# Optimization experiments

Hardware: AMD Instinct MI355X
Metric: run time of the kernel (lower is better)

Reference implementation:

```python
import jax, jax.numpy as jnp
import numpy as np

B, T, VOCAB_SZ, N_SPK = 64, 1024, 34, 128
D_TXT, D_SPK, H, N_MELS = 512, 64, 256, 80


def _lstm_params(key, in_dim, hid):
    k1, k2, k3, k4 = jax.random.split(key, 4)
    s = 1.0 / np.sqrt(hid)
    Wih = jax.random.uniform(k1, (4 * hid, in_dim), jnp.float32, -s, s)
    Whh = jax.random.uniform(k2, (4 * hid, hid), jnp.float32, -s, s)
    bih = jax.random.uniform(k3, (4 * hid,), jnp.float32, -s, s)
    bhh = jax.random.uniform(k4, (4 * hid,), jnp.float32, -s, s)
    return Wih, Whh, bih, bhh


def setup_inputs() -> dict:
    key = jax.random.key(0)
    ks = jax.random.split(key, 10)
    text_seq = jax.random.randint(ks[0], (B, T), 0, VOCAB_SZ)
    mel_spectrogram = jax.random.normal(ks[1], (B, T, N_MELS), jnp.float32)
    speaker_id = jax.random.randint(ks[2], (B,), 0, N_SPK)
    emb_text = jax.random.normal(ks[3], (VOCAB_SZ, D_TXT), jnp.float32)
    emb_text = emb_text.at[0].set(0.0)  # padding_idx=0
    emb_spk = jax.random.normal(ks[4], (N_SPK, D_SPK), jnp.float32)
    Wih_f, Whh_f, bih_f, bhh_f = _lstm_params(ks[5], D_TXT + D_SPK, H)
    Wih_b, Whh_b, bih_b, bhh_b = _lstm_params(ks[6], D_TXT + D_SPK, H)
    Wih_d, _Whh_d, bih_d, bhh_d = _lstm_params(ks[7], N_MELS + 2 * H, H)
    s = 1.0 / np.sqrt(H)
    Wfc = jax.random.uniform(ks[8], (N_MELS, H), jnp.float32, -s, s)
    bfc = jax.random.uniform(ks[9], (N_MELS,), jnp.float32, -s, s)
    return dict(text_seq=text_seq, mel_spectrogram=mel_spectrogram, speaker_id=speaker_id,
                emb_text=emb_text, emb_spk=emb_spk,
                Wih_f=Wih_f, Whh_f=Whh_f, bih_f=bih_f, bhh_f=bhh_f,
                Wih_b=Wih_b, Whh_b=Whh_b, bih_b=bih_b, bhh_b=bhh_b,
                Wih_d=Wih_d, bih_d=bih_d, bhh_d=bhh_d, Wfc=Wfc, bfc=bfc)


def _lstm_scan(xs, Wih, Whh, bih, bhh, reverse=False):
    # xs: [T, B, D] -> hs: [T, B, H] (PyTorch gate order i,f,g,o)
    nB, hid = xs.shape[1], Whh.shape[1]
    bias = bih + bhh
    def step(carry, x):
        h, c = carry
        g = x @ Wih.T + h @ Whh.T + bias
        i, f, gg, o = jnp.split(g, 4, axis=-1)
        c = jax.nn.sigmoid(f) * c + jax.nn.sigmoid(i) * jnp.tanh(gg)
        h = jax.nn.sigmoid(o) * jnp.tanh(c)
        return (h, c), h
    init = (jnp.zeros((nB, hid), xs.dtype), jnp.zeros((nB, hid), xs.dtype))
    _, hs = jax.lax.scan(step, init, xs, reverse=reverse)
    return hs


def reference(text_seq, mel_spectrogram, speaker_id, emb_text, emb_spk,
              Wih_f, Whh_f, bih_f, bhh_f, Wih_b, Whh_b, bih_b, bhh_b,
              Wih_d, bih_d, bhh_d, Wfc, bfc):
    text_embed = emb_text[text_seq]                       # [B, T, 512]
    spk = jnp.broadcast_to(emb_spk[speaker_id][:, None, :],
                           (text_seq.shape[0], text_seq.shape[1], emb_spk.shape[1]))
    enc_in = jnp.concatenate([text_embed, spk], axis=-1)  # [B, T, 576]
    xs = jnp.transpose(enc_in, (1, 0, 2))                 # time-major [T, B, 576]
    h_fwd = _lstm_scan(xs, Wih_f, Whh_f, bih_f, bhh_f)
    h_bwd = _lstm_scan(xs, Wih_b, Whh_b, bih_b, bhh_b, reverse=True)
    enc_out = jnp.concatenate([h_fwd, h_bwd], axis=-1)    # [T, B, 512]

    max_len = min(mel_spectrogram.shape[1], enc_out.shape[0])
    # Decoder: hidden state is reset (None) every step in the original, so
    # c = sigmoid(i)*tanh(g), h = sigmoid(o)*tanh(c); Whh contributes nothing.
    dbias = bih_d + bhh_d
    def dstep(prev_mel, e_t):
        x = jnp.concatenate([prev_mel, e_t], axis=-1)     # [B, 592]
        g = x @ Wih_d.T + dbias
        i, f, gg, o = jnp.split(g, 4, axis=-1)
        c = jax.nn.sigmoid(i) * jnp.tanh(gg)
        h = jax.nn.sigmoid(o) * jnp.tanh(c)
        out = h @ Wfc.T + bfc
        return out, out
    _, outs = jax.lax.scan(dstep, mel_spectrogram[:, 0, :], enc_out[: max_len - 1])
    return jnp.transpose(outs, (1, 0, 2))                 # [B, max_len-1, 80]
```

## Files before the change

kernel.cpp:

```cpp
#include <hip/hip_runtime.h>
#include <hip/hip_fp16.h>
#include <stdint.h>

#define T_SEQ 1024
#define NB    64
#define VOCAB 34
#define NSPK  128
#define DTXT  512
#define HID   256
#define NMEL  80
#define GROWS 1024
#define DROWS 768

typedef _Float16 f16;
typedef _Float16 f16x2 __attribute__((ext_vector_type(2)));
typedef _Float16 v8h __attribute__((ext_vector_type(8)));
typedef float v4f __attribute__((ext_vector_type(4)));

__device__ __forceinline__ float fdot2f(uint32_t a, uint32_t b, float c) {
  return __builtin_amdgcn_fdot2(__builtin_bit_cast(f16x2, a),
                                __builtin_bit_cast(f16x2, b), c, false);
}
__device__ __forceinline__ float sigm(float x) { return 1.0f / (1.0f + __expf(-x)); }
__device__ __forceinline__ float tanhf_fast(float x) {
  float e = __expf(2.0f * x);
  return 1.0f - 2.0f / (e + 1.0f);
}
__device__ __forceinline__ void bar_vperm() {
  asm volatile("s_waitcnt lgkmcnt(0)\n\ts_barrier" ::: "memory");
  __builtin_amdgcn_sched_barrier(0);
}


__global__ void k_tp(const float* __restrict__ Wf, const float* __restrict__ Wb,
                     const float* __restrict__ emb_text, float* __restrict__ TP) {
  int blk = blockIdx.x; int dir = blk / VOCAB; int v = blk - dir * VOCAB;
  const float* W = dir ? Wb : Wf;
  const float* e = emb_text + (size_t)v * DTXT;
  for (int r = threadIdx.x; r < GROWS; r += 256) {
    const float* wr = W + (size_t)r * 576;
    float a0 = 0, a1 = 0, a2 = 0, a3 = 0;
    for (int d = 0; d < DTXT; d += 4) {
      a0 += e[d] * wr[d];     a1 += e[d+1] * wr[d+1];
      a2 += e[d+2] * wr[d+2]; a3 += e[d+3] * wr[d+3];
    }
    TP[(size_t)(dir * VOCAB + v) * GROWS + r] = (a0 + a1) + (a2 + a3);
  }
}

__global__ void k_sp(const float* __restrict__ Wf, const float* __restrict__ Wb,
                     const float* __restrict__ bihf, const float* __restrict__ bhhf,
                     const float* __restrict__ bihb, const float* __restrict__ bhhb,
                     const float* __restrict__ emb_spk, float* __restrict__ SP) {
  int blk = blockIdx.x; int dir = blk >> 7; int s = blk & 127;
  const float* W  = dir ? Wb : Wf;
  const float* bi = dir ? bihb : bihf;
  const float* bh = dir ? bhhb : bhhf;
  const float* e  = emb_spk + (size_t)s * 64;
  for (int r = threadIdx.x; r < GROWS; r += 256) {
    const float* wr = W + (size_t)r * 576 + 512;
    float acc = bi[r] + bh[r];
    for (int d = 0; d < 64; ++d) acc += e[d] * wr[d];
    SP[(size_t)(dir * NSPK + s) * GROWS + r] = acc;
  }
}

__global__ void k_whh(const float* __restrict__ Whhf, const float* __restrict__ Whhb,
                      f16* __restrict__ WhhH) {
  int idx = blockIdx.x * 256 + threadIdx.x;
  if (idx < 2 * GROWS * HID) {
    int dir = idx >> 18; int rem = idx & (GROWS * HID - 1);
    WhhH[idx] = (f16)(dir ? Whhb[rem] : Whhf[rem]);
  }
}

__global__ void k_decw(const float* __restrict__ Wih_d, const float* __restrict__ bih_d,
                       const float* __restrict__ bhh_d,
                       f16* __restrict__ WmH, f16* __restrict__ WdH, float* __restrict__ dbias) {
  int r = blockIdx.x;
  int src = (r < 256) ? r : (r + 256);
  const float* w = Wih_d + (size_t)src * 592;
  for (int k = threadIdx.x; k < 592; k += 256) {
    float v = w[k];
    if (k < 80) WmH[(size_t)r * 80 + k] = (f16)v;
    else        WdH[(size_t)r * 512 + (k - 80)] = (f16)v;
  }
  if (threadIdx.x == 0) dbias[r] = bih_d[src] + bhh_d[src];
}

__global__ void k_misc(const float* __restrict__ Wfc, f16* __restrict__ WfcH) {
  int idx = blockIdx.x * 256 + threadIdx.x;
  if (idx < NMEL * HID) WfcH[idx] = (f16)Wfc[idx];
}

__launch_bounds__(512, 2)
__global__ void k_enc(const int* __restrict__ text_seq, const int* __restrict__ speaker_id,
                      const float* __restrict__ TP, const float* __restrict__ SP,
                      const uint32_t* __restrict__ WhhH_dw,
                      f16* __restrict__ Hh) {
  __shared__ __align__(16) uint4 wtail[16 * 512];
  __shared__ __align__(16) uint32_t hbuf[2][128];
  __shared__ float pp[4][256];
  __shared__ int tseq[T_SEQ];

  int wg = blockIdx.x;
  int dir = wg >> 6, b = wg & 63;
  int tid = threadIdx.x;
  int u = tid & 255, kh = tid >> 8;

  uint4 w0[12], w1[12], w2[12], w3[12];
  {
    const uint4* p0 = (const uint4*)(WhhH_dw + ((size_t)(dir << 10) + u      ) * 128 + (kh << 6));
    const uint4* p1 = (const uint4*)(WhhH_dw + ((size_t)(dir << 10) + u + 256) * 128 + (kh << 6));
    const uint4* p2 = (const uint4*)(WhhH_dw + ((size_t)(dir << 10) + u + 512) * 128 + (kh << 6));
    const uint4* p3 = (const uint4*)(WhhH_dw + ((size_t)(dir << 10) + u + 768) * 128 + (kh << 6));
    #pragma unroll
    for (int i = 0; i < 12; ++i) { w0[i] = p0[i]; w1[i] = p1[i]; w2[i] = p2[i]; w3[i] = p3[i]; }
    #pragma unroll
    for (int j = 0; j < 4; ++j) {
      wtail[(0 * 4 + j) * 512 + tid] = p0[12 + j];
      wtail[(1 * 4 + j) * 512 + tid] = p1[12 + j];
      wtail[(2 * 4 + j) * 512 + tid] = p2[12 + j];
      wtail[(3 * 4 + j) * 512 + tid] = p3[12 + j];
    }
  }
  for (int i = tid; i < T_SEQ; i += 512) tseq[i] = text_seq[b * T_SEQ + i];
  if (tid < 128) hbuf[0][tid] = 0u;
  float sp0 = 0, sp1 = 0, sp2 = 0, sp3 = 0;
  if (kh == 0) {
    int spk = speaker_id[b];
    sp0 = SP[(size_t)(dir * NSPK + spk) * GROWS + u];
    sp1 = SP[(size_t)(dir * NSPK + spk) * GROWS + u + 256];
    sp2 = SP[(size_t)(dir * NSPK + spk) * GROWS + u + 512];
    sp3 = SP[(size_t)(dir * NSPK + spk) * GROWS + u + 768];
  }
  const float* TPd = TP + (size_t)dir * VOCAB * GROWS;
  float c_state = 0.0f;
  __syncthreads();

  float x0 = 0, x1 = 0, x2 = 0, x3 = 0;
  if (kh == 0) {
    int v = tseq[dir ? (T_SEQ - 1) : 0];
    x0 = TPd[(size_t)v * GROWS + u];
    x1 = TPd[(size_t)v * GROWS + u + 256];
    x2 = TPd[(size_t)v * GROWS + u + 512];
    x3 = TPd[(size_t)v * GROWS + u + 768];
  }

  float h_keep = 0.0f; int t_keep = 0;
  for (int n = 0; n < T_SEQ; ++n) {
    int t = dir ? (T_SEQ - 1 - n) : n;
    float xn0 = 0, xn1 = 0, xn2 = 0, xn3 = 0;
    if (kh == 0) {
      if (n > 0)
        Hh[((size_t)(dir * T_SEQ + t_keep) * NB + b) * HID + u] = (f16)h_keep;
      int tn = dir ? (T_SEQ - 2 - n) : (n + 1);
      tn = tn < 0 ? 0 : (tn > T_SEQ - 1 ? T_SEQ - 1 : tn);
      int vn = tseq[tn];
      xn0 = TPd[(size_t)vn * GROWS + u];
      xn1 = TPd[(size_t)vn * GROWS + u + 256];
      xn2 = TPd[(size_t)vn * GROWS + u + 512];
      xn3 = TPd[(size_t)vn * GROWS + u + 768];
    }

    float i0 = 0, i1 = 0, f0 = 0, f1 = 0, g0 = 0, g1 = 0, o0 = 0, o1 = 0;
    const uint4* h4 = ((const uint4*)hbuf[n & 1]) + (kh << 4);
    #pragma unroll
    for (int c = 0; c < 12; ++c) {
      uint4 hv = h4[c];
      i0 = fdot2f(w0[c].x, hv.x, i0); f0 = fdot2f(w1[c].x, hv.x, f0);
      g0 = fdot2f(w2[c].x, hv.x, g0); o0 = fdot2f(w3[c].x, hv.x, o0);
      i1 = fdot2f(w0[c].y, hv.y, i1); f1 = fdot2f(w1[c].y, hv.y, f1);
      g1 = fdot2f(w2[c].y, hv.y, g1); o1 = fdot2f(w3[c].y, hv.y, o1);
      i0 = fdot2f(w0[c].z, hv.z, i0); f0 = fdot2f(w1[c].z, hv.z, f0);
      g0 = fdot2f(w2[c].z, hv.z, g0); o0 = fdot2f(w3[c].z, hv.z, o0);
      i1 = fdot2f(w0[c].w, hv.w, i1); f1 = fdot2f(w1[c].w, hv.w, f1);
      g1 = fdot2f(w2[c].w, hv.w, g1); o1 = fdot2f(w3[c].w, hv.w, o1);
    }
    #pragma unroll
    for (int j = 0; j < 4; ++j) {
      uint4 hv = h4[12 + j];
      uint4 t0v = wtail[(0 * 4 + j) * 512 + tid];
      uint4 t1v = wtail[(1 * 4 + j) * 512 + tid];
      uint4 t2v = wtail[(2 * 4 + j) * 512 + tid];
      uint4 t3v = wtail[(3 * 4 + j) * 512 + tid];
      i0 = fdot2f(t0v.x, hv.x, i0); f0 = fdot2f(t1v.x, hv.x, f0);
      g0 = fdot2f(t2v.x, hv.x, g0); o0 = fdot2f(t3v.x, hv.x, o0);
      i1 = fdot2f(t0v.y, hv.y, i1); f1 = fdot2f(t1v.y, hv.y, f1);
      g1 = fdot2f(t2v.y, hv.y, g1); o1 = fdot2f(t3v.y, hv.y, o1);
      i0 = fdot2f(t0v.z, hv.z, i0); f0 = fdot2f(t1v.z, hv.z, f0);
      g0 = fdot2f(t2v.z, hv.z, g0); o0 = fdot2f(t3v.z, hv.z, o0);
      i1 = fdot2f(t0v.w, hv.w, i1); f1 = fdot2f(t1v.w, hv.w, f1);
      g1 = fdot2f(t2v.w, hv.w, g1); o1 = fdot2f(t3v.w, hv.w, o1);
    }
    if (kh == 1) {
      pp[0][u] = i0 + i1;
      pp[1][u] = f0 + f1;
      pp[2][u] = g0 + g1;
      pp[3][u] = o0 + o1;
    }
    bar_vperm();

    if (kh == 0) {
      float gi = (i0 + i1) + pp[0][u] + x0 + sp0;
      float gf = (f0 + f1) + pp[1][u] + x1 + sp1;
      float gg = (g0 + g1) + pp[2][u] + x2 + sp2;
      float go = (o0 + o1) + pp[3][u] + x3 + sp3;
      c_state = sigm(gf) * c_state + sigm(gi) * tanhf_fast(gg);
      float h = sigm(go) * tanhf_fast(c_state);
      ((f16*)hbuf[(n + 1) & 1])[u] = (f16)h;
      h_keep = h; t_keep = t;
      x0 = xn0; x1 = xn1; x2 = xn2; x3 = xn3;
    }
    bar_vperm();
  }
  if (kh == 0)
    Hh[((size_t)(dir * T_SEQ + t_keep) * NB + b) * HID + u] = (f16)h_keep;
}

__launch_bounds__(256, 4)
__global__ void k_eproj(const uint32_t* __restrict__ Hdw, const uint32_t* __restrict__ WdH_dw,
                        const float* __restrict__ dbias, f16* __restrict__ E) {
  __shared__ __align__(16) uint32_t Asm[64][68];
  __shared__ __align__(16) uint32_t Wsm[64][68];
  int nt = blockIdx.x % 12;
  int t  = blockIdx.x / 12;
  int n0 = nt * 64;
  int tid = threadIdx.x;
  int wave = tid >> 6, lane = tid & 63;
  int lr = lane & 15, lg = lane >> 4;

  v4f acc0 = {0,0,0,0}, acc1 = {0,0,0,0}, acc2 = {0,0,0,0}, acc3 = {0,0,0,0};

  for (int ch = 0; ch < 4; ++ch) {
    int dirc = ch >> 1, koff = (ch & 1) * 64;
    {
      int bb = tid >> 2, p = tid & 3;
      const uint32_t* asrc = Hdw + ((size_t)(dirc * T_SEQ + t) * NB + bb) * 128 + koff + p * 4;
      const uint32_t* wsrc = WdH_dw + (size_t)(n0 + bb) * 256 + ch * 64 + p * 4;
      #pragma unroll
      for (int q = 0; q < 4; ++q) {
        *(uint4*)(&Asm[bb][p * 4 + q * 16]) = *(const uint4*)(asrc + q * 16);
        *(uint4*)(&Wsm[bb][p * 4 + q * 16]) = *(const uint4*)(wsrc + q * 16);
      }
    }
    __syncthreads();
    #pragma unroll
    for (int sub = 0; sub < 4; ++sub) {
      v8h af = __builtin_bit_cast(v8h, *(const uint4*)&Asm[wave * 16 + lr][sub * 16 + lg * 4]);
      v8h b0 = __builtin_bit_cast(v8h, *(const uint4*)&Wsm[ 0 + lr][sub * 16 + lg * 4]);
      v8h b1 = __builtin_bit_cast(v8h, *(const uint4*)&Wsm[16 + lr][sub * 16 + lg * 4]);
      v8h b2 = __builtin_bit_cast(v8h, *(const uint4*)&Wsm[32 + lr][sub * 16 + lg * 4]);
      v8h b3 = __builtin_bit_cast(v8h, *(const uint4*)&Wsm[48 + lr][sub * 16 + lg * 4]);
      acc0 = __builtin_amdgcn_mfma_f32_16x16x32_f16(af, b0, acc0, 0, 0, 0);
      acc1 = __builtin_amdgcn_mfma_f32_16x16x32_f16(af, b1, acc1, 0, 0, 0);
      acc2 = __builtin_amdgcn_mfma_f32_16x16x32_f16(af, b2, acc2, 0, 0, 0);
      acc3 = __builtin_amdgcn_mfma_f32_16x16x32_f16(af, b3, acc3, 0, 0, 0);
    }
    __syncthreads();
  }

  float db0 = dbias[n0 +  0 + lr];
  float db1 = dbias[n0 + 16 + lr];
  float db2 = dbias[n0 + 32 + lr];
  float db3 = dbias[n0 + 48 + lr];
  #pragma unroll
  for (int reg = 0; reg < 4; ++reg) {
    int m = wave * 16 + lg * 4 + reg;
    f16* Erow = E + ((size_t)t * NB + m) * DROWS + n0;
    Erow[ 0 + lr] = (f16)(acc0[reg] + db0);
    Erow[16 + lr] = (f16)(acc1[reg] + db1);
    Erow[32 + lr] = (f16)(acc2[reg] + db2);
    Erow[48 + lr] = (f16)(acc3[reg] + db3);
  }
}

__launch_bounds__(512, 2)
__global__ void k_dec(const float* __restrict__ mel, const f16* __restrict__ E,
                      const uint32_t* __restrict__ WmH_dw, const uint32_t* __restrict__ WfcH_dw,
                      const float* __restrict__ bfc, float* __restrict__ out) {
  __shared__ __align__(16) uint32_t pm[40];
  __shared__ __align__(16) uint32_t h_sm[128];
  __shared__ float pp[3][256];
  __shared__ __align__(16) uint4 Ebuf[2][16 * 96];

  int b = blockIdx.x;
  int tid = threadIdx.x;
  int u = tid & 255, kh = tid >> 8;

  uint4 wm0[5], wm1[5], wm2[5];
  {
    const uint4* p0 = (const uint4*)(WmH_dw + (size_t)(u      ) * 40) + kh * 5;
    const uint4* p1 = (const uint4*)(WmH_dw + (size_t)(u + 256) * 40) + kh * 5;
    const uint4* p2 = (const uint4*)(WmH_dw + (size_t)(u + 512) * 40) + kh * 5;
    #pragma unroll
    for (int k = 0; k < 5; ++k) { wm0[k] = p0[k]; wm1[k] = p1[k]; wm2[k] = p2[k]; }
  }
  int fr = (tid < 320) ? (tid >> 2) : 0;
  int q  = tid & 3;
  uint4 wfc[8];
  {
    const uint4* wp = (const uint4*)(WfcH_dw + (size_t)fr * 128) + q * 8;
    #pragma unroll
    for (int k = 0; k < 8; ++k) wfc[k] = wp[k];
  }
  float bfcv = bfc[fr];
  if (tid < 40) {
    float m0 = mel[(size_t)b * T_SEQ * NMEL + 2 * tid];
    float m1 = mel[(size_t)b * T_SEQ * NMEL + 2 * tid + 1];
    f16x2 v; v[0] = (f16)m0; v[1] = (f16)m1;
    pm[tid] = __builtin_bit_cast(uint32_t, v);
  }

  int srow = tid >> 5, scol = tid & 31;
  {
    const uint4* src = (const uint4*)(E + ((size_t)srow * NB + b) * DROWS);
    Ebuf[0][srow * 96 + scol     ] = src[scol];
    Ebuf[0][srow * 96 + scol + 32] = src[scol + 32];
    Ebuf[0][srow * 96 + scol + 64] = src[scol + 64];
  }
  __syncthreads();

  float o_keep = 0.0f;
  for (int t = 0; t < T_SEQ - 1; ++t) {
    int w = t >> 4, s = t & 15;
    if (t > 0 && tid < 320 && q == 0)
      out[((size_t)b * (T_SEQ - 1) + (t - 1)) * NMEL + fr] = o_keep;
    uint4 st0, st1, st2;
    bool do_stage = (s == 0) && (w < 63);
    if (do_stage) {
      int rr = (w + 1) * 16 + srow; if (rr > T_SEQ - 2) rr = T_SEQ - 2;
      const uint4* src = (const uint4*)(E + ((size_t)rr * NB + b) * DROWS);
      st0 = src[scol]; st1 = src[scol + 32]; st2 = src[scol + 64];
    }

    float a0 = 0, a1 = 0, a2 = 0;
    const uint4* pm4 = ((const uint4*)pm) + kh * 5;
    #pragma unroll
    for (int k = 0; k < 5; ++k) {
      uint4 hp = pm4[k];
      a0 = fdot2f(wm0[k].x, hp.x, a0); a1 = fdot2f(wm1[k].x, hp.x, a1); a2 = fdot2f(wm2[k].x, hp.x, a2);
      a0 = fdot2f(wm0[k].y, hp.y, a0); a1 = fdot2f(wm1[k].y, hp.y, a1); a2 = fdot2f(wm2[k].y, hp.y, a2);
      a0 = fdot2f(wm0[k].z, hp.z, a0); a1 = fdot2f(wm1[k].z, hp.z, a1); a2 = fdot2f(wm2[k].z, hp.z, a2);
      a0 = fdot2f(wm0[k].w, hp.w, a0); a1 = fdot2f(wm1[k].w, hp.w, a1); a2 = fdot2f(wm2[k].w, hp.w, a2);
    }
    if (kh == 1) { pp[0][u] = a0; pp[1][u] = a1; pp[2][u] = a2; }
    bar_vperm();

    if (kh == 0) {
      const f16* Erow = (const f16*)&Ebuf[w & 1][s * 96];
      float gi = a0 + pp[0][u] + (float)Erow[u];
      float gg = a1 + pp[1][u] + (float)Erow[u + 256];
      float go = a2 + pp[2][u] + (float)Erow[u + 512];
      float cc = sigm(gi) * tanhf_fast(gg);
      float h  = sigm(go) * tanhf_fast(cc);
      ((f16*)h_sm)[u] = (f16)h;
    }
    if (do_stage) {
      Ebuf[(w + 1) & 1][srow * 96 + scol     ] = st0;
      Ebuf[(w + 1) & 1][srow * 96 + scol + 32] = st1;
      Ebuf[(w + 1) & 1][srow * 96 + scol + 64] = st2;
    }
    bar_vperm();

    if (tid < 320) {
      const uint4* hrow = ((const uint4*)h_sm) + q * 8;
      float s0 = 0, s1 = 0, s2 = 0, s3 = 0;
      #pragma unroll
      for (int kk = 0; kk < 8; ++kk) {
        uint4 hq = hrow[kk];
        s0 = fdot2f(wfc[kk].x, hq.x, s0); s1 = fdot2f(wfc[kk].y, hq.y, s1);
        s2 = fdot2f(wfc[kk].z, hq.z, s2); s3 = fdot2f(wfc[kk].w, hq.w, s3);
      }
      float sv = (s0 + s1) + (s2 + s3);
      sv += __shfl_xor(sv, 1);
      sv += __shfl_xor(sv, 2);
      if (q == 0) {
        float o = sv + bfcv;
        o_keep = o;
        ((f16*)pm)[fr] = (f16)o;
      }
    }
    bar_vperm();
  }
  if (tid < 320 && q == 0)
    out[((size_t)b * (T_SEQ - 1) + (T_SEQ - 2)) * NMEL + fr] = o_keep;
}

extern "C" void kernel_launch(void* const* d_in, const int* in_sizes, int n_in,
                              void* d_out, int out_size, void* d_ws, size_t ws_size,
                              hipStream_t stream) {
  const int*   text_seq   = (const int*)d_in[0];
  const float* mel        = (const float*)d_in[1];
  const int*   speaker_id = (const int*)d_in[2];
  const float* emb_text   = (const float*)d_in[3];
  const float* emb_spk    = (const float*)d_in[4];
  const float* Wih_f = (const float*)d_in[5];
  const float* Whh_f = (const float*)d_in[6];
  const float* bih_f = (const float*)d_in[7];
  const float* bhh_f = (const float*)d_in[8];
  const float* Wih_b = (const float*)d_in[9];
  const float* Whh_b = (const float*)d_in[10];
  const float* bih_b = (const float*)d_in[11];
  const float* bhh_b = (const float*)d_in[12];
  const float* Wih_d = (const float*)d_in[13];
  const float* bih_d = (const float*)d_in[14];
  const float* bhh_d = (const float*)d_in[15];
  const float* Wfc   = (const float*)d_in[16];
  const float* bfc   = (const float*)d_in[17];
  float* out = (float*)d_out;

  char* base = (char*)d_ws;
  size_t off = 0;
  auto take = [&](size_t n) -> char* {
    off = (off + 255) & ~(size_t)255;
    char* r = base + off;
    off += n;
    return r;
  };
  float*        TP    = (float*)take((size_t)2 * VOCAB * GROWS * 4);
  float*        SP    = (float*)take((size_t)2 * NSPK * GROWS * 4);
  f16*          WhhH  = (f16*)take((size_t)2 * GROWS * HID * 2);
  f16*          WmH   = (f16*)take((size_t)DROWS * 80 * 2);
  f16*          WdH   = (f16*)take((size_t)DROWS * 512 * 2);
  f16*          WfcH  = (f16*)take((size_t)NMEL * HID * 2);
  float*        dbias = (float*)take((size_t)DROWS * 4);
  f16*          Hh    = (f16*)take((size_t)2 * T_SEQ * NB * HID * 2);
  f16*          E     = (f16*)take((size_t)(T_SEQ - 1) * NB * DROWS * 2);
  if (off > ws_size) return;

  k_tp  <<<2 * VOCAB, 256, 0, stream>>>(Wih_f, Wih_b, emb_text, TP);
  k_sp  <<<2 * NSPK, 256, 0, stream>>>(Wih_f, Wih_b, bih_f, bhh_f, bih_b, bhh_b, emb_spk, SP);
  k_whh <<<2048, 256, 0, stream>>>(Whh_f, Whh_b, WhhH);
  k_decw<<<DROWS, 256, 0, stream>>>(Wih_d, bih_d, bhh_d, WmH, WdH, dbias);
  k_misc<<<80, 256, 0, stream>>>(Wfc, WfcH);
  k_enc <<<128, 512, 0, stream>>>(text_seq, speaker_id, TP, SP,
                                  (const uint32_t*)WhhH, Hh);
  k_eproj<<<(T_SEQ - 1) * 12, 256, 0, stream>>>((const uint32_t*)Hh,
                                                (const uint32_t*)WdH, dbias, E);
  k_dec <<<NB, 512, 0, stream>>>(mel, E, (const uint32_t*)WmH,
                                 (const uint32_t*)WfcH, bfc, out);
}
```

Baseline: 2.846 ms.

## Process two batch rows per decoder block and vectorize input-projection precompute

```diff
diff --git a/kernel.cpp b/kernel.cpp
--- a/kernel.cpp
+++ b/kernel.cpp
@@ -36,13 +36,15 @@
                      const float* __restrict__ emb_text, float* __restrict__ TP) {
   int blk = blockIdx.x; int dir = blk / VOCAB; int v = blk - dir * VOCAB;
   const float* W = dir ? Wb : Wf;
-  const float* e = emb_text + (size_t)v * DTXT;
+  const float4* e4 = (const float4*)(emb_text + (size_t)v * DTXT);
   for (int r = threadIdx.x; r < GROWS; r += 256) {
-    const float* wr = W + (size_t)r * 576;
+    const float4* w4 = (const float4*)(W + (size_t)r * 576);
     float a0 = 0, a1 = 0, a2 = 0, a3 = 0;
-    for (int d = 0; d < DTXT; d += 4) {
-      a0 += e[d] * wr[d];     a1 += e[d+1] * wr[d+1];
-      a2 += e[d+2] * wr[d+2]; a3 += e[d+3] * wr[d+3];
+    #pragma unroll 4
+    for (int d = 0; d < DTXT / 4; ++d) {
+      float4 ev = e4[d], wv = w4[d];
+      a0 += ev.x * wv.x; a1 += ev.y * wv.y;
+      a2 += ev.z * wv.z; a3 += ev.w * wv.w;
     }
     TP[(size_t)(dir * VOCAB + v) * GROWS + r] = (a0 + a1) + (a2 + a3);
   }
@@ -56,12 +58,17 @@
   const float* W  = dir ? Wb : Wf;
   const float* bi = dir ? bihb : bihf;
   const float* bh = dir ? bhhb : bhhf;
-  const float* e  = emb_spk + (size_t)s * 64;
+  const float4* e4 = (const float4*)(emb_spk + (size_t)s * 64);
   for (int r = threadIdx.x; r < GROWS; r += 256) {
-    const float* wr = W + (size_t)r * 576 + 512;
-    float acc = bi[r] + bh[r];
-    for (int d = 0; d < 64; ++d) acc += e[d] * wr[d];
-    SP[(size_t)(dir * NSPK + s) * GROWS + r] = acc;
+    const float4* w4 = (const float4*)(W + (size_t)r * 576 + 512);
+    float a0 = 0, a1 = 0, a2 = 0, a3 = 0;
+    #pragma unroll
+    for (int d = 0; d < 16; ++d) {
+      float4 ev = e4[d], wv = w4[d];
+      a0 += ev.x * wv.x; a1 += ev.y * wv.y;
+      a2 += ev.z * wv.z; a3 += ev.w * wv.w;
+    }
+    SP[(size_t)(dir * NSPK + s) * GROWS + r] = bi[r] + bh[r] + (a0 + a1) + (a2 + a3);
   }
 }
 
@@ -279,22 +286,22 @@
 __global__ void k_dec(const float* __restrict__ mel, const f16* __restrict__ E,
                       const uint32_t* __restrict__ WmH_dw, const uint32_t* __restrict__ WfcH_dw,
                       const float* __restrict__ bfc, float* __restrict__ out) {
-  __shared__ __align__(16) uint32_t pm[40];
-  __shared__ __align__(16) uint32_t h_sm[128];
-  __shared__ float pp[3][256];
-  __shared__ __align__(16) uint4 Ebuf[2][16 * 96];
-
-  int b = blockIdx.x;
+  __shared__ __align__(16) uint32_t pm[2][40];
+  __shared__ __align__(16) uint32_t h_sm[2][128];
+  __shared__ __align__(16) uint4 Ebuf[2][2][16 * 96];
+
+  int b2 = blockIdx.x;
   int tid = threadIdx.x;
-  int u = tid & 255, kh = tid >> 8;
-
-  uint4 wm0[5], wm1[5], wm2[5];
+  int u = tid & 255, hb = tid >> 8;
+  int b = b2 + 32 * hb;
+
+  uint4 wm0[10], wm1[10], wm2[10];
   {
-    const uint4* p0 = (const uint4*)(WmH_dw + (size_t)(u      ) * 40) + kh * 5;
-    const uint4* p1 = (const uint4*)(WmH_dw + (size_t)(u + 256) * 40) + kh * 5;
-    const uint4* p2 = (const uint4*)(WmH_dw + (size_t)(u + 512) * 40) + kh * 5;
-    #pragma unroll
-    for (int k = 0; k < 5; ++k) { wm0[k] = p0[k]; wm1[k] = p1[k]; wm2[k] = p2[k]; }
+    const uint4* p0 = (const uint4*)(WmH_dw + (size_t)(u      ) * 40);
+    const uint4* p1 = (const uint4*)(WmH_dw + (size_t)(u + 256) * 40);
+    const uint4* p2 = (const uint4*)(WmH_dw + (size_t)(u + 512) * 40);
+    #pragma unroll
+    for (int k = 0; k < 10; ++k) { wm0[k] = p0[k]; wm1[k] = p1[k]; wm2[k] = p2[k]; }
   }
   int fr = (tid < 320) ? (tid >> 2) : 0;
   int q  = tid & 3;
@@ -305,86 +312,103 @@
     for (int k = 0; k < 8; ++k) wfc[k] = wp[k];
   }
   float bfcv = bfc[fr];
-  if (tid < 40) {
-    float m0 = mel[(size_t)b * T_SEQ * NMEL + 2 * tid];
-    float m1 = mel[(size_t)b * T_SEQ * NMEL + 2 * tid + 1];
+  if (tid < 80) {
+    int hbi = tid / 40, idx = tid - 40 * hbi;
+    int bb = b2 + 32 * hbi;
+    float m0 = mel[(size_t)bb * T_SEQ * NMEL + 2 * idx];
+    float m1 = mel[(size_t)bb * T_SEQ * NMEL + 2 * idx + 1];
     f16x2 v; v[0] = (f16)m0; v[1] = (f16)m1;
-    pm[tid] = __builtin_bit_cast(uint32_t, v);
+    pm[hbi][idx] = __builtin_bit_cast(uint32_t, v);
   }
 
   int srow = tid >> 5, scol = tid & 31;
-  {
-    const uint4* src = (const uint4*)(E + ((size_t)srow * NB + b) * DROWS);
-    Ebuf[0][srow * 96 + scol     ] = src[scol];
-    Ebuf[0][srow * 96 + scol + 32] = src[scol + 32];
-    Ebuf[0][srow * 96 + scol + 64] = src[scol + 64];
+  #pragma unroll
+  for (int hbs = 0; hbs < 2; ++hbs) {
+    const uint4* src = (const uint4*)(E + ((size_t)srow * NB + b2 + 32 * hbs) * DROWS);
+    Ebuf[0][hbs][srow * 96 + scol     ] = src[scol];
+    Ebuf[0][hbs][srow * 96 + scol + 32] = src[scol + 32];
+    Ebuf[0][hbs][srow * 96 + scol + 64] = src[scol + 64];
   }
   __syncthreads();
 
-  float o_keep = 0.0f;
+  float o_keepA = 0.0f, o_keepB = 0.0f;
   for (int t = 0; t < T_SEQ - 1; ++t) {
     int w = t >> 4, s = t & 15;
-    if (t > 0 && tid < 320 && q == 0)
-      out[((size_t)b * (T_SEQ - 1) + (t - 1)) * NMEL + fr] = o_keep;
-    uint4 st0, st1, st2;
+    if (t > 0 && tid < 320 && q == 0) {
+      out[((size_t)(b2     ) * (T_SEQ - 1) + (t - 1)) * NMEL + fr] = o_keepA;
+      out[((size_t)(b2 + 32) * (T_SEQ - 1) + (t - 1)) * NMEL + fr] = o_keepB;
+    }
+    uint4 stA0, stA1, stA2, stB0, stB1, stB2;
     bool do_stage = (s == 0) && (w < 63);
     if (do_stage) {
       int rr = (w + 1) * 16 + srow; if (rr > T_SEQ - 2) rr = T_SEQ - 2;
-      const uint4* src = (const uint4*)(E + ((size_t)rr * NB + b) * DROWS);
-      st0 = src[scol]; st1 = src[scol + 32]; st2 = src[scol + 64];
-    }
-
-    float a0 = 0, a1 = 0, a2 = 0;
-    const uint4* pm4 = ((const uint4*)pm) + kh * 5;
-    #pragma unroll
-    for (int k = 0; k < 5; ++k) {
+      const uint4* sa = (const uint4*)(E + ((size_t)rr * NB + b2     ) * DROWS);
+      const uint4* sb = (const uint4*)(E + ((size_t)rr * NB + b2 + 32) * DROWS);
+      stA0 = sa[scol]; stA1 = sa[scol + 32]; stA2 = sa[scol + 64];
+      stB0 = sb[scol]; stB1 = sb[scol + 32]; stB2 = sb[scol + 64];
+    }
+
+    float a0a = 0, a0b = 0, a1a = 0, a1b = 0, a2a = 0, a2b = 0;
+    const uint4* pm4 = (const uint4*)pm[hb];
+    #pragma unroll
+    for (int k = 0; k < 10; k += 2) {
       uint4 hp = pm4[k];
-      a0 = fdot2f(wm0[k].x, hp.x, a0); a1 = fdot2f(wm1[k].x, hp.x, a1); a2 = fdot2f(wm2[k].x, hp.x, a2);
-      a0 = fdot2f(wm0[k].y, hp.y, a0); a1 = fdot2f(wm1[k].y, hp.y, a1); a2 = fdot2f(wm2[k].y, hp.y, a2);
-      a0 = fdot2f(wm0[k].z, hp.z, a0); a1 = fdot2f(wm1[k].z, hp.z, a1); a2 = fdot2f(wm2[k].z, hp.z, a2);
-      a0 = fdot2f(wm0[k].w, hp.w, a0); a1 = fdot2f(wm1[k].w, hp.w, a1); a2 = fdot2f(wm2[k].w, hp.w, a2);
-    }
-    if (kh == 1) { pp[0][u] = a0; pp[1][u] = a1; pp[2][u] = a2; }
-    bar_vperm();
-
-    if (kh == 0) {
-      const f16* Erow = (const f16*)&Ebuf[w & 1][s * 96];
-      float gi = a0 + pp[0][u] + (float)Erow[u];
-      float gg = a1 + pp[1][u] + (float)Erow[u + 256];
-      float go = a2 + pp[2][u] + (float)Erow[u + 512];
+      a0a = fdot2f(wm0[k].x, hp.x, a0a); a1a = fdot2f(wm1[k].x, hp.x, a1a); a2a = fdot2f(wm2[k].x, hp.x, a2a);
+      a0a = fdot2f(wm0[k].y, hp.y, a0a); a1a = fdot2f(wm1[k].y, hp.y, a1a); a2a = fdot2f(wm2[k].y, hp.y, a2a);
+      a0a = fdot2f(wm0[k].z, hp.z, a0a); a1a = fdot2f(wm1[k].z, hp.z, a1a); a2a = fdot2f(wm2[k].z, hp.z, a2a);
+      a0a = fdot2f(wm0[k].w, hp.w, a0a); a1a = fdot2f(wm1[k].w, hp.w, a1a); a2a = fdot2f(wm2[k].w, hp.w, a2a);
+      uint4 hq = pm4[k + 1];
+      a0b = fdot2f(wm0[k+1].x, hq.x, a0b); a1b = fdot2f(wm1[k+1].x, hq.x, a1b); a2b = fdot2f(wm2[k+1].x, hq.x, a2b);
+      a0b = fdot2f(wm0[k+1].y, hq.y, a0b); a1b = fdot2f(wm1[k+1].y, hq.y, a1b); a2b = fdot2f(wm2[k+1].y, hq.y, a2b);
+      a0b = fdot2f(wm0[k+1].z, hq.z, a0b); a1b = fdot2f(wm1[k+1].z, hq.z, a1b); a2b = fdot2f(wm2[k+1].z, hq.z, a2b);
+      a0b = fdot2f(wm0[k+1].w, hq.w, a0b); a1b = fdot2f(wm1[k+1].w, hq.w, a1b); a2b = fdot2f(wm2[k+1].w, hq.w, a2b);
+    }
+    {
+      const f16* Erow = (const f16*)&Ebuf[w & 1][hb][s * 96];
+      float gi = (a0a + a0b) + (float)Erow[u];
+      float gg = (a1a + a1b) + (float)Erow[u + 256];
+      float go = (a2a + a2b) + (float)Erow[u + 512];
       float cc = sigm(gi) * tanhf_fast(gg);
       float h  = sigm(go) * tanhf_fast(cc);
-      ((f16*)h_sm)[u] = (f16)h;
+      ((f16*)h_sm[hb])[u] = (f16)h;
     }
     if (do_stage) {
-      Ebuf[(w + 1) & 1][srow * 96 + scol     ] = st0;
-      Ebuf[(w + 1) & 1][srow * 96 + scol + 32] = st1;
-      Ebuf[(w + 1) & 1][srow * 96 + scol + 64] = st2;
+      Ebuf[(w + 1) & 1][0][srow * 96 + scol     ] = stA0;
+      Ebuf[(w + 1) & 1][0][srow * 96 + scol + 32] = stA1;
+      Ebuf[(w + 1) & 1][0][srow * 96 + scol + 64] = stA2;
+      Ebuf[(w + 1) & 1][1][srow * 96 + scol     ] = stB0;
+      Ebuf[(w + 1) & 1][1][srow * 96 + scol + 32] = stB1;
+      Ebuf[(w + 1) & 1][1][srow * 96 + scol + 64] = stB2;
     }
     bar_vperm();
 
     if (tid < 320) {
-      const uint4* hrow = ((const uint4*)h_sm) + q * 8;
-      float s0 = 0, s1 = 0, s2 = 0, s3 = 0;
       #pragma unroll
-      for (int kk = 0; kk < 8; ++kk) {
-        uint4 hq = hrow[kk];
-        s0 = fdot2f(wfc[kk].x, hq.x, s0); s1 = fdot2f(wfc[kk].y, hq.y, s1);
-        s2 = fdot2f(wfc[kk].z, hq.z, s2); s3 = fdot2f(wfc[kk].w, hq.w, s3);
+      for (int hbs = 0; hbs < 2; ++hbs) {
+        const uint4* hrow = ((const uint4*)h_sm[hbs]) + q * 8;
+        float s0 = 0, s1 = 0, s2 = 0, s3 = 0;
+        #pragma unroll
+        for (int kk = 0; kk < 8; ++kk) {
+          uint4 hq = hrow[kk];
+          s0 = fdot2f(wfc[kk].x, hq.x, s0); s1 = fdot2f(wfc[kk].y, hq.y, s1);
+          s2 = fdot2f(wfc[kk].z, hq.z, s2); s3 = fdot2f(wfc[kk].w, hq.w, s3);
+        }
+        float sv = (s0 + s1) + (s2 + s3);
+        sv += __shfl_xor(sv, 1);
+        sv += __shfl_xor(sv, 2);
+        if (q == 0) {
+          float o = sv + bfcv;
+          if (hbs == 0) o_keepA = o; else o_keepB = o;
+          ((f16*)pm[hbs])[fr] = (f16)o;
+        }
       }
-      float sv = (s0 + s1) + (s2 + s3);
-      sv += __shfl_xor(sv, 1);
-      sv += __shfl_xor(sv, 2);
-      if (q == 0) {
-        float o = sv + bfcv;
-        o_keep = o;
-        ((f16*)pm)[fr] = (f16)o;
-      }
     }
     bar_vperm();
   }
-  if (tid < 320 && q == 0)
-    out[((size_t)b * (T_SEQ - 1) + (T_SEQ - 2)) * NMEL + fr] = o_keep;
+  if (tid < 320 && q == 0) {
+    out[((size_t)(b2     ) * (T_SEQ - 1) + (T_SEQ - 2)) * NMEL + fr] = o_keepA;
+    out[((size_t)(b2 + 32) * (T_SEQ - 1) + (T_SEQ - 2)) * NMEL + fr] = o_keepB;
+  }
 }
 
 extern "C" void kernel_launch(void* const* d_in, const int* in_sizes, int n_in,
@@ -438,6 +462,6 @@
                                   (const uint32_t*)WhhH, Hh);
   k_eproj<<<(T_SEQ - 1) * 12, 256, 0, stream>>>((const uint32_t*)Hh,
                                                 (const uint32_t*)WdH, dbias, E);
-  k_dec <<<NB, 512, 0, stream>>>(mel, E, (const uint32_t*)WmH,
+  k_dec <<<32, 512, 0, stream>>>(mel, E, (const uint32_t*)WmH,
                                  (const uint32_t*)WfcH, bfc, out);
 }
```

New measurement: 3.451 ms. 21.3% more time.
